# Performance work log

Measured on AMD Instinct MI355X. Metric: run time of the kernel, lower is better.

## Reference

```python
import jax, jax.numpy as jnp
import numpy as np

B, S, D_IN, D_Q, D_V, H = 2, 2048, 1024, 1024, 1024, 16
HD_Q, HD_V = D_Q // H, D_V // H
SCALE = float(D_Q) ** 0.5  # source scales by sqrt(d_q), NOT sqrt(head_dim)


def setup_inputs() -> dict:
    key = jax.random.key(0)
    k1, k2, k3, k4, k5 = jax.random.split(key, 5)
    return {
        "x": jax.random.normal(k1, (B, S, D_IN), dtype=jnp.float32),
        "w_q": jax.random.normal(k2, (D_IN, D_Q), dtype=jnp.float32),
        "w_k": jax.random.normal(k3, (D_IN, D_Q), dtype=jnp.float32),
        "w_v": jax.random.normal(k4, (D_IN, D_V), dtype=jnp.float32),
        "W_o": jax.random.normal(k5, (D_IN, D_V), dtype=jnp.float32),
    }


def reference(x, w_q, w_k, w_v, W_o):
    b, s, _ = x.shape
    # projections: [b, s, d]
    q = x @ w_q
    k = x @ w_k
    v = x @ w_v
    # split heads -> [b, h, s, hd]
    Q = q.reshape(b, s, H, HD_Q).transpose(0, 2, 1, 3)
    K = k.reshape(b, s, H, HD_Q).transpose(0, 2, 1, 3)
    V = v.reshape(b, s, H, HD_V).transpose(0, 2, 1, 3)
    # full [b, h, s, s] score matrix (naive attention, as in source)
    scores = jnp.einsum("bhqd,bhkd->bhqk", Q, K)
    # FAITHFUL QUIRK: source applies softmax over dim=0 (batch axis)
    attn = jax.nn.softmax(scores / SCALE, axis=0)
    vals = jnp.einsum("bhqk,bhkd->bhqd", attn, V)
    vals = vals.transpose(0, 2, 1, 3).reshape(b, s, D_V)
    return vals @ W_o
```

## Files before the change

### kernel.cpp

```cpp
#include <hip/hip_runtime.h>


typedef _Float16 f16;
typedef __attribute__((ext_vector_type(8))) _Float16 f16x8;
typedef __attribute__((ext_vector_type(4))) _Float16 f16x4;
typedef __attribute__((ext_vector_type(4))) float f32x4;

#define MFMA16(a,b,c) __builtin_amdgcn_mfma_f32_16x16x32_f16(a,b,c,0,0,0)
#define GLD16(gp, lp) __builtin_amdgcn_global_load_lds(                         \
    (const __attribute__((address_space(1))) void*)(gp),                        \
    (__attribute__((address_space(3))) void*)(lp), 16, 0, 0)

__global__ __launch_bounds__(256) void prep(const float* __restrict__ x,
                                            const float* __restrict__ w0, const float* __restrict__ w1,
                                            const float* __restrict__ w2, const float* __restrict__ w3,
                                            f16* __restrict__ xh,
                                            f16* __restrict__ o0, f16* __restrict__ o1,
                                            f16* __restrict__ o2, f16* __restrict__ o3) {
    const int bb = blockIdx.x;
    const int tid = threadIdx.x;
    if (bb >= 1024) {
        int i = (bb - 1024) * 256 + tid;
        float4 v = ((const float4*)x)[i];
        f16x4 h;
        h[0] = (f16)v.x; h[1] = (f16)v.y; h[2] = (f16)v.z; h[3] = (f16)v.w;
        *(f16x4*)(xh + (long)i * 4) = h;
        return;
    }
    const float* w; f16* o;
    switch (bb & 3) {
        case 0: w = w0; o = o0; break;
        case 1: w = w1; o = o1; break;
        case 2: w = w2; o = o2; break;
        default: w = w3; o = o3; break;
    }
    __shared__ alignas(16) f16 t[64][72];
    const int d0 = ((bb >> 2) & 15) * 64, j0 = (bb >> 6) * 64;
    #pragma unroll
    for (int it = 0; it < 4; ++it) {
        int idx = it * 256 + tid;
        int row = idx >> 4, c4 = idx & 15;
        float4 v = *(const float4*)(w + (long)(d0 + row) * 1024 + j0 + c4 * 4);
        f16x4 h;
        h[0] = (f16)v.x; h[1] = (f16)v.y; h[2] = (f16)v.z; h[3] = (f16)v.w;
        *(f16x4*)&t[row][c4 * 4] = h;
    }
    __syncthreads();
    #pragma unroll
    for (int it = 0; it < 4; ++it) {
        int idx = it * 256 + tid;
        int jr = idx >> 4, d4 = idx & 15;
        f16x4 h;
        #pragma unroll
        for (int m = 0; m < 4; ++m) h[m] = t[d4 * 4 + m][jr];
        *(f16x4*)(o + (long)(j0 + jr) * 1024 + d0 + d4 * 4) = h;
    }
}

__global__ __launch_bounds__(256, 2) void gemm_qkv(const f16* __restrict__ A,
                                                   const f16* __restrict__ Wt,
                                                   f16* __restrict__ Qg,
                                                   f16* __restrict__ Kg,
                                                   f16* __restrict__ Vtg) {
    __shared__ alignas(16) f16 smem[17408];
    f16* As = smem;
    f16* Bs = smem + 8192;
    const int tid = threadIdx.x;
    const int wave = tid >> 6, lane = tid & 63;
    const int l15 = lane & 15, lq = lane >> 4;
    const int sw = l15 & 7;
    const int m0 = blockIdx.x * 128, n0 = blockIdx.y * 128;
    const int wr = (wave >> 1) * 64, wc = (wave & 1) * 64;
    const int r8 = lane >> 3;
    const int swc8 = ((lane & 7) ^ r8) * 8;

    f32x4 acc[4][4] = {};

    for (int kt = 0; kt < 16; ++kt) {
        __syncthreads();
        #pragma unroll
        for (int i = 0; i < 4; ++i) {
            GLD16(A  + (long)(m0 + wave * 32 + i * 8 + r8) * 1024 + kt * 64 + swc8, As + (wave * 32 + i * 8) * 64);
            GLD16(Wt + (long)(n0 + wave * 32 + i * 8 + r8) * 1024 + kt * 64 + swc8, Bs + (wave * 32 + i * 8) * 64);
        }
        __syncthreads();
        #pragma unroll
        for (int s2 = 0; s2 < 2; ++s2) {
            const int rc = ((s2 * 4 + lq) ^ sw) << 3;
            f16x8 af[4], bf[4];
            #pragma unroll
            for (int i = 0; i < 4; ++i) af[i] = *(const f16x8*)&As[(wr + i * 16 + l15) * 64 + rc];
            #pragma unroll
            for (int j = 0; j < 4; ++j) bf[j] = *(const f16x8*)&Bs[(wc + j * 16 + l15) * 64 + rc];
            #pragma unroll
            for (int i = 0; i < 4; ++i)
                #pragma unroll
                for (int j = 0; j < 4; ++j)
                    acc[i][j] = MFMA16(af[i], bf[j], acc[i][j]);
        }
    }

    const int sel = n0 >> 10;
    const int nb = n0 - (sel << 10);

    if (sel < 2) {
        f16* dst = sel == 0 ? Qg : Kg;
        const float qs = sel == 0 ? (m0 >= 2048 ? 0.045084219f : -0.045084219f) : 1.0f;
        __syncthreads();
        #pragma unroll
        for (int i = 0; i < 4; ++i)
            #pragma unroll
            for (int j = 0; j < 4; ++j) {
                int row0 = wr + i * 16 + lq * 4;
                int colb = wc + j * 16 + l15;
                int chunk = colb >> 3, sub = colb & 7;
                #pragma unroll
                for (int r = 0; r < 4; ++r) {
                    int row = row0 + r;
                    smem[row * 128 + ((chunk ^ (row & 7)) << 3) + sub] = (f16)(acc[i][j][r] * qs);
                }
            }
        __syncthreads();
        #pragma unroll
        for (int e = 0; e < 8; ++e) {
            int id = e * 256 + tid;
            int row = id >> 4, c = id & 15;
            f16x8 v = *(const f16x8*)&smem[row * 128 + ((c ^ (row & 7)) << 3)];
            int gr = m0 + row, b = gr >> 11, s = gr & 2047;
            int gc = nb + c * 8, hh = gc >> 6, hd = gc & 63;
            *(f16x8*)(dst + (long)((b * 16 + hh) * 2048 + s) * 64 + hd) = v;
        }
    } else {
        __syncthreads();
        #pragma unroll
        for (int i = 0; i < 4; ++i)
            #pragma unroll
            for (int j = 0; j < 4; ++j) {
                int row0 = wr + i * 16 + lq * 4;
                int c    = wc + j * 16 + l15;
                #pragma unroll
                for (int r = 0; r < 4; ++r)
                    smem[c * 136 + row0 + r] = (f16)acc[i][j][r];
            }
        __syncthreads();
        const int b = m0 >> 11, sbase = m0 & 2047;
        #pragma unroll
        for (int e = 0; e < 8; ++e) {
            int id = e * 256 + tid;
            int c = id >> 4, sc8 = (id & 15) * 8;
            f16x8 v = *(const f16x8*)&smem[c * 136 + sc8];
            int gc = nb + c, hh = gc >> 6, hd = gc & 63;
            *(f16x8*)(Vtg + (long)((b * 16 + hh) * 64 + hd) * 2048 + sbase + sc8) = v;
        }
    }
}

__global__ __launch_bounds__(256) void usum(const f16* __restrict__ Vtg, f16* __restrict__ u) {
    const int h = blockIdx.x;
    const int tid = threadIdx.x;
    const int row = tid >> 2, seg = tid & 3;
    const f16* p = Vtg + ((long)(16 + h) * 64 + row) * 2048 + seg * 8;
    float s = 0.0f;
    #pragma unroll 4
    for (int j = 0; j < 64; ++j) {
        f16x8 v = *(const f16x8*)(p + j * 32);
        #pragma unroll
        for (int m = 0; m < 8; ++m) s += (float)v[m];
    }
    s += __shfl_xor(s, 1);
    s += __shfl_xor(s, 2);
    if (seg == 0) u[h * 64 + row] = (f16)s;
}

__global__ __launch_bounds__(256, 2) void gemm_out(const f16* __restrict__ A0,
                                                   const f16* __restrict__ A1,
                                                   const f16* __restrict__ u,
                                                   const f16* __restrict__ Bt,
                                                   float* __restrict__ outp) {
    __shared__ alignas(16) f16 As[64][72];
    __shared__ alignas(16) f16 Bs[128][64];
    const int tid = threadIdx.x;
    const int wave = tid >> 6, lane = tid & 63;
    const int l15 = lane & 15, lq = lane >> 4;
    const int sw = l15 & 7;
    const int bid = blockIdx.x;
    const int m0 = ((bid >> 6) * 8 + (bid & 7)) * 64;
    const int n0 = ((bid >> 3) & 7) * 128;
    const bool b1 = m0 >= 2048;
    const int wr = (wave >> 1) * 32, wc = (wave & 1) * 64;
    const int r8 = lane >> 3;
    const int swc8 = ((lane & 7) ^ r8) * 8;

    f32x4 acc[2][4] = {};

    for (int kt = 0; kt < 16; ++kt) {
        __syncthreads();
        #pragma unroll
        for (int it = 0; it < 2; ++it) {
            int idx = it * 256 + tid;
            int row = idx >> 3, c = idx & 7;
            f16x8 a = *(const f16x8*)(A0 + (long)(m0 + row) * 1024 + kt * 64 + c * 8)
                    + *(const f16x8*)(A1 + (long)(m0 + row) * 1024 + kt * 64 + c * 8);
            if (b1) a += *(const f16x8*)(u + kt * 64 + c * 8);
            *(f16x8*)&As[row][c * 8] = a;
        }
        #pragma unroll
        for (int i = 0; i < 4; ++i)
            GLD16(Bt + (long)(n0 + wave * 32 + i * 8 + r8) * 1024 + kt * 64 + swc8, &Bs[wave * 32 + i * 8][0]);
        __syncthreads();
        #pragma unroll
        for (int s2 = 0; s2 < 2; ++s2) {
            const int rc = ((s2 * 4 + lq) ^ sw) << 3;
            f16x8 af[2], bf[4];
            #pragma unroll
            for (int i = 0; i < 2; ++i) af[i] = *(const f16x8*)&As[wr + i * 16 + l15][s2 * 32 + lq * 8];
            #pragma unroll
            for (int j = 0; j < 4; ++j) bf[j] = *(const f16x8*)&Bs[wc + j * 16 + l15][rc];
            #pragma unroll
            for (int i = 0; i < 2; ++i)
                #pragma unroll
                for (int j = 0; j < 4; ++j)
                    acc[i][j] = MFMA16(af[i], bf[j], acc[i][j]);
        }
    }

    #pragma unroll
    for (int i = 0; i < 2; ++i)
        #pragma unroll
        for (int j = 0; j < 4; ++j) {
            int gr0 = m0 + wr + i * 16 + lq * 4;
            int gc  = n0 + wc + j * 16 + l15;
            #pragma unroll
            for (int r = 0; r < 4; ++r)
                outp[(long)(gr0 + r) * 1024 + gc] = acc[i][j][r];
        }
}

__global__ __launch_bounds__(256, 2) void attention_kernel(const f16* __restrict__ Qg,
                                                           const f16* __restrict__ Kg,
                                                           const f16* __restrict__ Vtg,
                                                           f16* __restrict__ vals0,
                                                           f16* __restrict__ vals1) {
    __shared__ alignas(16) f16 Ks [2][2][64][64];
    __shared__ alignas(16) f16 Vts[2][2][64][64];
    __shared__ alignas(16) f16 Ps [4][32][64];
    const int tid = threadIdx.x;
    const int wave = tid >> 6, lane = tid & 63;
    const int l15 = lane & 15, lq = lane >> 4;
    const int sw = l15 & 7;

    const int bid = blockIdx.x;
    const int xcd = bid & 7, sl = bid >> 3;
    const int h  = xcd * 2 + (sl & 1);
    const int qt = (sl >> 1) & 15, ks = sl >> 5;
    const int q0 = qt * 128, kt0 = ks * 16;
    f16* vals = ks ? vals1 : vals0;
    const int qr = q0 + wave * 32;

    f16x8 qfr[2][2][2];
    #pragma unroll
    for (int b2 = 0; b2 < 2; ++b2)
        #pragma unroll
        for (int qq = 0; qq < 2; ++qq)
            #pragma unroll
            for (int s2 = 0; s2 < 2; ++s2)
                qfr[b2][qq][s2] = *(const f16x8*)(Qg + (long)((b2 * 16 + h) * 2048 + qr + qq * 16 + l15) * 64
                                                  + s2 * 32 + lq * 8);

    f32x4 acc[2][2][4] = {};

    const int tb = wave & 1;
    const int r8 = lane >> 3;
    const int swc8 = ((lane & 7) ^ r8) * 8;
    const f16* kbase = Kg  + (long)((tb * 16 + h) * 2048 + kt0 * 64) * 64 + r8 * 64 + swc8;
    const f16* vbase = Vtg + (long)((tb * 16 + h) * 64 + r8) * 2048 + kt0 * 64 + swc8;

    auto stage = [&](int kt, int buf) {
        if (wave < 2) {
            const f16* g = kbase + kt * 4096;
            f16* l = &Ks[buf][tb][0][0];
            #pragma unroll
            for (int i = 0; i < 8; ++i) GLD16(g + i * 512, l + i * 512);
        } else {
            const f16* g = vbase + kt * 64;
            f16* l = &Vts[buf][tb][0][0];
            #pragma unroll
            for (int i = 0; i < 8; ++i) GLD16(g + (long)i * 8 * 2048, l + i * 512);
        }
    };

    stage(0, 0);
    for (int kt = 0; kt < 16; ++kt) {
        const int cur = kt & 1;
        __syncthreads();
        if (kt < 15) stage(kt + 1, cur ^ 1);

        f16x4 pp[2][4];
        #pragma unroll
        for (int kf = 0; kf < 4; ++kf) {
            f32x4 D[2] = {};
            #pragma unroll
            for (int s2 = 0; s2 < 2; ++s2) {
                const int rc = ((s2 * 4 + lq) ^ sw) << 3;
                f16x8 a0 = *(const f16x8*)&Ks[cur][0][kf * 16 + l15][rc];
                f16x8 a1 = *(const f16x8*)&Ks[cur][1][kf * 16 + l15][rc];
                #pragma unroll
                for (int qq = 0; qq < 2; ++qq) {
                    D[qq] = MFMA16(a0, qfr[0][qq][s2], D[qq]);
                    D[qq] = MFMA16(a1, qfr[1][qq][s2], D[qq]);
                }
            }
            #pragma unroll
            for (int qq = 0; qq < 2; ++qq)
                #pragma unroll
                for (int r = 0; r < 4; ++r) {
                    float e = __builtin_amdgcn_exp2f(D[qq][r]);
                    float p = __builtin_amdgcn_rcpf(1.0f + e);
                    pp[qq][kf][r] = (f16)p;
                }
        }

        const int pwsub = (lq & 1) << 2;
        #pragma unroll
        for (int qq = 0; qq < 2; ++qq)
            #pragma unroll
            for (int kf = 0; kf < 4; ++kf)
                *(f16x4*)&Ps[wave][qq * 16 + l15][(((2 * kf + (lq >> 1)) ^ sw) << 3) + pwsub]
                    = pp[qq][kf];

        #pragma unroll
        for (int s2 = 0; s2 < 2; ++s2) {
            const int rc = ((s2 * 4 + lq) ^ sw) << 3;
            f16x8 pf[2], vf0[4], vf1[4];
            #pragma unroll
            for (int qq = 0; qq < 2; ++qq)
                pf[qq] = *(const f16x8*)&Ps[wave][qq * 16 + l15][rc];
            #pragma unroll
            for (int hf = 0; hf < 4; ++hf) {
                vf0[hf] = *(const f16x8*)&Vts[cur][0][hf * 16 + l15][rc];
                vf1[hf] = *(const f16x8*)&Vts[cur][1][hf * 16 + l15][rc];
            }
            #pragma unroll
            for (int qq = 0; qq < 2; ++qq)
                #pragma unroll
                for (int hf = 0; hf < 4; ++hf) {
                    acc[0][qq][hf] = MFMA16(pf[qq], vf0[hf], acc[0][qq][hf]);
                    acc[1][qq][hf] = MFMA16(pf[qq], vf1[hf], acc[1][qq][hf]);
                }
        }
    }

    #pragma unroll
    for (int b2 = 0; b2 < 2; ++b2)
        #pragma unroll
        for (int qq = 0; qq < 2; ++qq)
            #pragma unroll
            for (int hf = 0; hf < 4; ++hf)
                #pragma unroll
                for (int r = 0; r < 4; ++r) {
                    float v = acc[b2][qq][hf][r];
                    vals[(long)(b2 * 2048 + qr + qq * 16 + lq * 4 + r) * 1024 + h * 64 + hf * 16 + l15]
                        = (f16)(b2 ? -v : v);
                }
}

extern "C" void kernel_launch(void* const* d_in, const int* in_sizes, int n_in,
                              void* d_out, int out_size, void* d_ws, size_t ws_size,
                              hipStream_t stream) {
    const float* x  = (const float*)d_in[0];
    const float* wq = (const float*)d_in[1];
    const float* wk = (const float*)d_in[2];
    const float* wv = (const float*)d_in[3];
    const float* wo = (const float*)d_in[4];

    char* ws = (char*)d_ws;
    f16* xh    = (f16*)(ws);
    f16* wqT   = (f16*)(ws + 8388608);
    f16* wkT   = (f16*)(ws + 10485760);
    f16* wvT   = (f16*)(ws + 12582912);
    f16* woT   = (f16*)(ws + 14680064);
    f16* Qg    = (f16*)(ws + 16777216);
    f16* Kg    = (f16*)(ws + 25165824);
    f16* Vtg   = (f16*)(ws + 33554432);
    f16* vals1 = (f16*)(ws + 41943040);
    f16* vals0 = xh;
    f16* u     = wqT;
    (void)ws_size; (void)in_sizes; (void)n_in; (void)out_size;

    prep<<<5120, 256, 0, stream>>>(x, wq, wk, wv, wo, xh, wqT, wkT, wvT, woT);

    gemm_qkv<<<dim3(32, 24), 256, 0, stream>>>(xh, wqT, Qg, Kg, Vtg);

    usum<<<16, 256, 0, stream>>>(Vtg, u);

    attention_kernel<<<512, 256, 0, stream>>>(Qg, Kg, Vtg, vals0, vals1);

    gemm_out<<<512, 256, 0, stream>>>(vals0, vals1, u, woT, (float*)d_out);
}
```

Before: 194.9 us.

## Fuse V column-sum into QKV GEMM epilogue and single-buffer attention tiles for occupancy

Removes the separate usum kernel by accumulating per-column sums of V for batch 1 inside the gemm_qkv epilogue, using float atomics into a zeroed buffer. gemm_out reads the float u and converts it to f16. The attention kernel drops double-buffering of K/V tiles, halving their LDS, and raises launch bounds to 3 blocks per CU. The aim is higher occupancy and one less kernel launch, at the cost of losing load/compute overlap in attention and adding atomics plus a memset.

```diff
diff --git a/kernel.cpp b/kernel.cpp
--- a/kernel.cpp
+++ b/kernel.cpp
@@ -61,7 +61,8 @@
                                                    const f16* __restrict__ Wt,
                                                    f16* __restrict__ Qg,
                                                    f16* __restrict__ Kg,
-                                                   f16* __restrict__ Vtg) {
+                                                   f16* __restrict__ Vtg,
+                                                   float* __restrict__ u) {
     __shared__ alignas(16) f16 smem[17408];
     f16* As = smem;
     f16* Bs = smem + 8192;
@@ -131,6 +132,21 @@
             *(f16x8*)(dst + (long)((b * 16 + hh) * 2048 + s) * 64 + hd) = v;
         }
     } else {
+        const int b = m0 >> 11, sbase = m0 & 2047;
+        if (b) {
+            #pragma unroll
+            for (int j = 0; j < 4; ++j) {
+                float cs = 0.0f;
+                #pragma unroll
+                for (int i = 0; i < 4; ++i)
+                    #pragma unroll
+                    for (int r = 0; r < 4; ++r)
+                        cs += (float)(f16)acc[i][j][r];
+                cs += __shfl_xor(cs, 16);
+                cs += __shfl_xor(cs, 32);
+                if (lq == 0) atomicAdd(&u[nb + wc + j * 16 + l15], cs);
+            }
+        }
         __syncthreads();
         #pragma unroll
         for (int i = 0; i < 4; ++i)
@@ -143,7 +159,6 @@
                     smem[c * 136 + row0 + r] = (f16)acc[i][j][r];
             }
         __syncthreads();
-        const int b = m0 >> 11, sbase = m0 & 2047;
         #pragma unroll
         for (int e = 0; e < 8; ++e) {
             int id = e * 256 + tid;
@@ -155,26 +170,9 @@
     }
 }
 
-__global__ __launch_bounds__(256) void usum(const f16* __restrict__ Vtg, f16* __restrict__ u) {
-    const int h = blockIdx.x;
-    const int tid = threadIdx.x;
-    const int row = tid >> 2, seg = tid & 3;
-    const f16* p = Vtg + ((long)(16 + h) * 64 + row) * 2048 + seg * 8;
-    float s = 0.0f;
-    #pragma unroll 4
-    for (int j = 0; j < 64; ++j) {
-        f16x8 v = *(const f16x8*)(p + j * 32);
-        #pragma unroll
-        for (int m = 0; m < 8; ++m) s += (float)v[m];
-    }
-    s += __shfl_xor(s, 1);
-    s += __shfl_xor(s, 2);
-    if (seg == 0) u[h * 64 + row] = (f16)s;
-}
-
 __global__ __launch_bounds__(256, 2) void gemm_out(const f16* __restrict__ A0,
                                                    const f16* __restrict__ A1,
-                                                   const f16* __restrict__ u,
+                                                   const float* __restrict__ u,
                                                    const f16* __restrict__ Bt,
                                                    float* __restrict__ outp) {
     __shared__ alignas(16) f16 As[64][72];
@@ -201,7 +199,13 @@
             int row = idx >> 3, c = idx & 7;
             f16x8 a = *(const f16x8*)(A0 + (long)(m0 + row) * 1024 + kt * 64 + c * 8)
                     + *(const f16x8*)(A1 + (long)(m0 + row) * 1024 + kt * 64 + c * 8);
-            if (b1) a += *(const f16x8*)(u + kt * 64 + c * 8);
+            if (b1) {
+                const float* up = u + kt * 64 + c * 8;
+                f16x8 uv;
+                #pragma unroll
+                for (int m = 0; m < 8; ++m) uv[m] = (f16)up[m];
+                a += uv;
+            }
             *(f16x8*)&As[row][c * 8] = a;
         }
         #pragma unroll
@@ -236,13 +240,13 @@
         }
 }
 
-__global__ __launch_bounds__(256, 2) void attention_kernel(const f16* __restrict__ Qg,
+__global__ __launch_bounds__(256, 3) void attention_kernel(const f16* __restrict__ Qg,
                                                            const f16* __restrict__ Kg,
                                                            const f16* __restrict__ Vtg,
                                                            f16* __restrict__ vals0,
                                                            f16* __restrict__ vals1) {
-    __shared__ alignas(16) f16 Ks [2][2][64][64];
-    __shared__ alignas(16) f16 Vts[2][2][64][64];
+    __shared__ alignas(16) f16 Ks [2][64][64];
+    __shared__ alignas(16) f16 Vts[2][64][64];
     __shared__ alignas(16) f16 Ps [4][32][64];
     const int tid = threadIdx.x;
     const int wave = tid >> 6, lane = tid & 63;
@@ -275,25 +279,20 @@
     const f16* kbase = Kg  + (long)((tb * 16 + h) * 2048 + kt0 * 64) * 64 + r8 * 64 + swc8;
     const f16* vbase = Vtg + (long)((tb * 16 + h) * 64 + r8) * 2048 + kt0 * 64 + swc8;
 
-    auto stage = [&](int kt, int buf) {
+    for (int kt = 0; kt < 16; ++kt) {
+        __syncthreads();
         if (wave < 2) {
             const f16* g = kbase + kt * 4096;
-            f16* l = &Ks[buf][tb][0][0];
+            f16* l = &Ks[tb][0][0];
             #pragma unroll
             for (int i = 0; i < 8; ++i) GLD16(g + i * 512, l + i * 512);
         } else {
             const f16* g = vbase + kt * 64;
-            f16* l = &Vts[buf][tb][0][0];
+            f16* l = &Vts[tb][0][0];
             #pragma unroll
             for (int i = 0; i < 8; ++i) GLD16(g + (long)i * 8 * 2048, l + i * 512);
         }
-    };
-
-    stage(0, 0);
-    for (int kt = 0; kt < 16; ++kt) {
-        const int cur = kt & 1;
-        __syncthreads();
-        if (kt < 15) stage(kt + 1, cur ^ 1);
+        __syncthreads();
 
         f16x4 pp[2][4];
         #pragma unroll
@@ -302,8 +301,8 @@
             #pragma unroll
             for (int s2 = 0; s2 < 2; ++s2) {
                 const int rc = ((s2 * 4 + lq) ^ sw) << 3;
-                f16x8 a0 = *(const f16x8*)&Ks[cur][0][kf * 16 + l15][rc];
-                f16x8 a1 = *(const f16x8*)&Ks[cur][1][kf * 16 + l15][rc];
+                f16x8 a0 = *(const f16x8*)&Ks[0][kf * 16 + l15][rc];
+                f16x8 a1 = *(const f16x8*)&Ks[1][kf * 16 + l15][rc];
                 #pragma unroll
                 for (int qq = 0; qq < 2; ++qq) {
                     D[qq] = MFMA16(a0, qfr[0][qq][s2], D[qq]);
@@ -337,8 +336,8 @@
                 pf[qq] = *(const f16x8*)&Ps[wave][qq * 16 + l15][rc];
             #pragma unroll
             for (int hf = 0; hf < 4; ++hf) {
-                vf0[hf] = *(const f16x8*)&Vts[cur][0][hf * 16 + l15][rc];
-                vf1[hf] = *(const f16x8*)&Vts[cur][1][hf * 16 + l15][rc];
+                vf0[hf] = *(const f16x8*)&Vts[0][hf * 16 + l15][rc];
+                vf1[hf] = *(const f16x8*)&Vts[1][hf * 16 + l15][rc];
             }
             #pragma unroll
             for (int qq = 0; qq < 2; ++qq)
@@ -374,24 +373,24 @@
     const float* wo = (const float*)d_in[4];
 
     char* ws = (char*)d_ws;
-    f16* xh    = (f16*)(ws);
-    f16* wqT   = (f16*)(ws + 8388608);
-    f16* wkT   = (f16*)(ws + 10485760);
-    f16* wvT   = (f16*)(ws + 12582912);
-    f16* woT   = (f16*)(ws + 14680064);
-    f16* Qg    = (f16*)(ws + 16777216);
-    f16* Kg    = (f16*)(ws + 25165824);
-    f16* Vtg   = (f16*)(ws + 33554432);
-    f16* vals1 = (f16*)(ws + 41943040);
-    f16* vals0 = xh;
-    f16* u     = wqT;
+    f16*   xh    = (f16*)(ws);
+    f16*   wqT   = (f16*)(ws + 8388608);
+    f16*   wkT   = (f16*)(ws + 10485760);
+    f16*   wvT   = (f16*)(ws + 12582912);
+    f16*   woT   = (f16*)(ws + 14680064);
+    f16*   Qg    = (f16*)(ws + 16777216);
+    f16*   Kg    = (f16*)(ws + 25165824);
+    f16*   Vtg   = (f16*)(ws + 33554432);
+    f16*   vals1 = (f16*)(ws + 41943040);
+    float* u     = (float*)(ws + 50331648);
+    f16*   vals0 = xh;
     (void)ws_size; (void)in_sizes; (void)n_in; (void)out_size;
 
+    hipMemsetAsync(u, 0, 1024 * sizeof(float), stream);
+
     prep<<<5120, 256, 0, stream>>>(x, wq, wk, wv, wo, xh, wqT, wkT, wvT, woT);
 
-    gemm_qkv<<<dim3(32, 24), 256, 0, stream>>>(xh, wqT, Qg, Kg, Vtg);
-
-    usum<<<16, 256, 0, stream>>>(Vtg, u);
+    gemm_qkv<<<dim3(32, 24), 256, 0, stream>>>(xh, wqT, Qg, Kg, Vtg, u);
 
     attention_kernel<<<512, 256, 0, stream>>>(Qg, Kg, Vtg, vals0, vals1);
 
```

New measurement: 189.8 us. -2.6%, faster.
